# Kernel tuning notes

Measured on AMD Instinct MI355X. Metric: run time of the kernel, lower is better.

The kernel has to match this reference:

```python
import jax, jax.numpy as jnp
import numpy as np

B, T, C, H = 4, 1024, 768, 12
HD = C // H  # 64
EPS = 1e-5

def setup_inputs() -> dict:
    key = jax.random.key(0)
    ks = jax.random.split(key, 6)
    s = 0.02
    return {
        "x": jax.random.normal(ks[0], (B, T, C), jnp.float32),
        "ln1_w": jnp.ones((C,), jnp.float32),
        "w_attn": jax.random.normal(ks[1], (C, 3 * C), jnp.float32) * s,
        "w_pos": jax.random.normal(ks[2], (C, C), jnp.float32) * s,
        "w_cproj": jax.random.normal(ks[3], (C, C), jnp.float32) * s,
        "ln2_w": jnp.ones((C,), jnp.float32),
        "w_fc": jax.random.normal(ks[4], (C, 4 * C), jnp.float32) * s,
        "w_mproj": jax.random.normal(ks[5], (4 * C, C), jnp.float32) * s,
    }

def _layernorm(x, w):
    m = jnp.mean(x, axis=-1, keepdims=True)
    v = jnp.mean(jnp.square(x - m), axis=-1, keepdims=True)
    return (x - m) * jax.lax.rsqrt(v + EPS) * w

def _rpe_table(dtype):
    # sinusoidal table over relative distances [-(T-1), T-1] -> [2T-1, HD]
    inv_freq = 1.0 / (10000.0 ** (jnp.arange(0, HD, 2, dtype=jnp.float32) / HD))
    dist = jnp.arange(-(T - 1), T, dtype=jnp.float32)
    freqs = dist[:, None] * inv_freq[None, :]
    return jnp.concatenate([jnp.sin(freqs), jnp.cos(freqs)], axis=-1).astype(dtype)

def reference(x, ln1_w, w_attn, w_pos, w_cproj, ln2_w, w_fc, w_mproj):
    # ---- attention branch ----
    h = _layernorm(x, ln1_w)
    qkv = h @ w_attn                                 # [B,T,3C]
    q, k, v = jnp.split(qkv, 3, axis=-1)
    q = q.reshape(B, T, H, HD).transpose(0, 2, 1, 3)  # [B,H,T,HD]
    k = k.reshape(B, T, H, HD).transpose(0, 2, 1, 3)
    v = v.reshape(B, T, H, HD).transpose(0, 2, 1, 3)
    # note: the original also computes p = c_pos(x) but never uses it (dead code)

    # relative position embeddings gathered to [T,T,HD]
    idx = jnp.arange(T)
    rel = jnp.clip(idx[:, None] - idx[None, :], -(T - 1), T - 1) + (T - 1)
    rpe = _rpe_table(q.dtype)[rel]                    # [T,T,HD]

    scale = 1.0 / np.sqrt(HD)
    att = (jnp.einsum('bhid,bhjd->bhij', q, k)
           + jnp.einsum('bhid,ijd->bhij', q, rpe)) * scale
    causal = idx[:, None] >= idx[None, :]             # [T,T] lower-tri
    att = jnp.where(causal, att, -jnp.inf)
    att = jax.nn.softmax(att, axis=-1)
    y = jnp.einsum('bhij,bhjd->bhid', att, v)         # [B,H,T,HD]
    y = y.transpose(0, 2, 1, 3).reshape(B, T, C) @ w_cproj
    x = x + y

    # ---- MLP branch ----
    h2 = _layernorm(x, ln2_w)
    m = jax.nn.gelu(h2 @ w_fc, approximate=False) @ w_mproj
    return x + m
```

## Files before the change

kernel.cpp:

```cpp
#include <hip/hip_runtime.h>
#include <math.h>

typedef __attribute__((ext_vector_type(8))) short bf16x8;
typedef __attribute__((ext_vector_type(4))) float f32x4;
typedef __attribute__((ext_vector_type(16))) float f32x16;
typedef __attribute__((ext_vector_type(4))) unsigned u32x4;

__device__ inline short f2bf(float f) {
  unsigned u = __builtin_bit_cast(unsigned, f);
  u = u + 0x7fffu + ((u >> 16) & 1u);
  return (short)(u >> 16);
}
__device__ inline float bf2f(short s) {
  return __builtin_bit_cast(float, ((unsigned)(unsigned short)s) << 16);
}
__device__ inline unsigned cvt_pk_bf16(float lo, float hi) {
  unsigned r;
  asm("v_cvt_pk_bf16_f32 %0, %1, %2" : "=v"(r) : "v"(lo), "v"(hi));
  return r;
}

__device__ inline void gload16(const short* g, short* l) {
  __builtin_amdgcn_global_load_lds(
      (const __attribute__((address_space(1))) unsigned*)g,
      (__attribute__((address_space(3))) unsigned*)l, 16, 0, 0);
}

__global__ __launch_bounds__(256) void wtrans_all(
    const float* __restrict__ wa, const float* __restrict__ wc,
    const float* __restrict__ wf, const float* __restrict__ wm,
    short* __restrict__ oa, short* __restrict__ oc,
    short* __restrict__ of, short* __restrict__ om) {
  __shared__ float tile[32][33];
  int blk = blockIdx.x;
  const float* in; short* out; int K, N, bx;
  if (blk < 1728)      { in = wa; out = oa; K = 768;  N = 2304; bx = 72; }
  else if (blk < 2304) { blk -= 1728; in = wc; out = oc; K = 768;  N = 768;  bx = 24; }
  else if (blk < 4608) { blk -= 2304; in = wf; out = of; K = 768;  N = 3072; bx = 96; }
  else                 { blk -= 4608; in = wm; out = om; K = 3072; N = 768;  bx = 24; }
  const int n0 = (blk % bx) * 32, k0 = (blk / bx) * 32;
  const int tx = threadIdx.x & 31, ty = threadIdx.x >> 5;
  #pragma unroll
  for (int r = ty; r < 32; r += 8)
    tile[r][tx] = in[(size_t)(k0 + r) * N + n0 + tx];
  __syncthreads();
  #pragma unroll
  for (int r = ty; r < 32; r += 8)
    out[(size_t)(n0 + r) * K + k0 + tx] = f2bf(tile[tx][r]);
}

__global__ __launch_bounds__(256) void qprime_kernel(
    const short* __restrict__ qkv, short* __restrict__ qpr,
    short* __restrict__ ktab) {
  const int idx = blockIdx.x * 256 + threadIdx.x;
  const int cc = idx & 31;
  const int row = idx >> 5;
  const int i = row & 1023, bh = row >> 10;
  const int b = bh / 12, h = bh % 12;
  const float invf = exp2f(-(float)cc * (13.287712379549449f / 32.0f));
  const float ang = (float)i * invf;
  float si, co;
  __sincosf(ang, &si, &co);
  if (bh == 0) {
    ktab[i * 64 + cc]      = f2bf(co);
    ktab[i * 64 + 32 + cc] = f2bf(si);
  }
  const short* q = qkv + (size_t)(b * 1024 + i) * 2304 + h * 64;
  const float qs = bf2f(q[cc]), qc = bf2f(q[32 + cc]);
  qpr[(size_t)row * 64 + cc]      = f2bf(qs * si + qc * co);
  qpr[(size_t)row * 64 + 32 + cc] = f2bf(qc * si - qs * co);
}

__global__ __launch_bounds__(256) void ln_kernel(
    const float* __restrict__ x, const float* __restrict__ w,
    short* __restrict__ out) {
  const int row = blockIdx.x, tid = threadIdx.x;
  const float* xr = x + (size_t)row * 768;
  float v0 = xr[tid], v1 = xr[tid + 256], v2 = xr[tid + 512];
  float s = v0 + v1 + v2;
  #pragma unroll
  for (int o = 1; o < 64; o <<= 1) s += __shfl_xor(s, o);
  __shared__ float red[8];
  const int wv = tid >> 6;
  if ((tid & 63) == 0) red[wv] = s;
  __syncthreads();
  const float mean = (red[0] + red[1] + red[2] + red[3]) * (1.0f / 768.0f);
  v0 -= mean; v1 -= mean; v2 -= mean;
  float q = v0 * v0 + v1 * v1 + v2 * v2;
  #pragma unroll
  for (int o = 1; o < 64; o <<= 1) q += __shfl_xor(q, o);
  if ((tid & 63) == 0) red[4 + wv] = q;
  __syncthreads();
  const float var = (red[4] + red[5] + red[6] + red[7]) * (1.0f / 768.0f);
  const float inv = 1.0f / sqrtf(var + 1e-5f);
  out[(size_t)row * 768 + tid]       = f2bf(v0 * inv * w[tid]);
  out[(size_t)row * 768 + tid + 256] = f2bf(v1 * inv * w[tid + 256]);
  out[(size_t)row * 768 + tid + 512] = f2bf(v2 * inv * w[tid + 512]);
}

__global__ __launch_bounds__(256) void vtrans_kernel(
    const short* __restrict__ qkv, short* __restrict__ vT) {
  __shared__ short tile[64][65];
  const int blk = blockIdx.x;
  const int bh = blk >> 4, t0 = (blk & 15) * 64;
  const int b = bh / 12, h = bh % 12;
  const int tx = threadIdx.x & 63, ty = threadIdx.x >> 6;
  const short* src = qkv + (size_t)(b * 1024 + t0) * 2304 + 1536 + h * 64;
  #pragma unroll
  for (int r = ty; r < 64; r += 4)
    tile[r][tx] = src[(size_t)r * 2304 + tx];
  __syncthreads();
  short* dst = vT + (size_t)bh * 64 * 1024 + t0;
  #pragma unroll
  for (int r = ty; r < 64; r += 4)
    dst[(size_t)r * 1024 + tx] = tile[tx][r];
}

template <int EPI, int BM, int BN>
__global__ __launch_bounds__(256) void gemm_bt(
    const short* __restrict__ A, const short* __restrict__ Bt,
    const float* __restrict__ res, float* __restrict__ outF,
    short* __restrict__ outB, int M, int N, int K, int lda, int ldb) {
  __shared__ __align__(16) short As[2][BM * 32];
  __shared__ __align__(16) short Bs[2][BN * 32];
  constexpr int WM = BM / 2, WN = BN / 2;
  constexpr int MI = WM / 16, NJ = WN / 16;
  const int tid = threadIdx.x;
  const int w = tid >> 6, lane = tid & 63;
  const int m0 = blockIdx.y * BM, n0 = blockIdx.x * BN;
  const int wm = (w >> 1) * WM, wn = (w & 1) * WN;
  const int lr = lane >> 2;
  const int lc = (lane & 3) * 8;
  if constexpr (EPI == 3) {
    A += (size_t)blockIdx.z * K;
    Bt += (size_t)blockIdx.z * K;
    outF += (size_t)blockIdx.z * M * N;
  }
  f32x4 acc[MI][NJ];
  #pragma unroll
  for (int i = 0; i < MI; i++)
    #pragma unroll
    for (int j = 0; j < NJ; j++)
      #pragma unroll
      for (int r = 0; r < 4; r++) acc[i][j][r] = 0.0f;

  const int nt = K / 32;
  #pragma unroll
  for (int p = 0; p < BM / 64; ++p)
    gload16(A + (size_t)(m0 + p * 64 + w * 16 + lr) * lda + lc,
            &As[0][p * 2048 + w * 512]);
  #pragma unroll
  for (int p = 0; p < BN / 64; ++p)
    gload16(Bt + (size_t)(n0 + p * 64 + w * 16 + lr) * ldb + lc,
            &Bs[0][p * 2048 + w * 512]);
  __syncthreads();

  for (int t = 0; t < nt; ++t) {
    const int cur = t & 1;
    if (t + 1 < nt) {
      const int kt = (t + 1) * 32;
      #pragma unroll
      for (int p = 0; p < BM / 64; ++p)
        gload16(A + (size_t)(m0 + p * 64 + w * 16 + lr) * lda + kt + lc,
                &As[cur ^ 1][p * 2048 + w * 512]);
      #pragma unroll
      for (int p = 0; p < BN / 64; ++p)
        gload16(Bt + (size_t)(n0 + p * 64 + w * 16 + lr) * ldb + kt + lc,
                &Bs[cur ^ 1][p * 2048 + w * 512]);
    }
    bf16x8 af[MI], bfr[NJ];
    #pragma unroll
    for (int i = 0; i < MI; i++)
      af[i] = *(const bf16x8*)&As[cur][(wm + i * 16 + (lane & 15)) * 32 + (lane >> 4) * 8];
    #pragma unroll
    for (int j = 0; j < NJ; j++)
      bfr[j] = *(const bf16x8*)&Bs[cur][(wn + j * 16 + (lane & 15)) * 32 + (lane >> 4) * 8];
    #pragma unroll
    for (int i = 0; i < MI; i++)
      #pragma unroll
      for (int j = 0; j < NJ; j++)
        acc[i][j] = __builtin_amdgcn_mfma_f32_16x16x32_bf16(af[i], bfr[j],
                                                            acc[i][j], 0, 0, 0);
    __syncthreads();
  }
  const int r0 = (lane >> 4) * 4, cl = lane & 15;
  #pragma unroll
  for (int i = 0; i < MI; i++) {
    #pragma unroll
    for (int j = 0; j < NJ; j++) {
      const int gm = m0 + wm + i * 16 + r0;
      const int gn = n0 + wn + j * 16 + cl;
      #pragma unroll
      for (int r = 0; r < 4; r++) {
        const size_t idx = (size_t)(gm + r) * N + gn;
        const float v = acc[i][j][r];
        if constexpr (EPI == 0) {
          outB[idx] = f2bf(v);
        } else if constexpr (EPI == 1) {
          outF[idx] = res[idx] + v;
        } else if constexpr (EPI == 2) {
          outB[idx] = f2bf(0.5f * v * (1.0f + erff(v * 0.70710678118f)));
        } else {
          outF[idx] = v;
        }
      }
    }
  }
}

__global__ __launch_bounds__(256) void reduce_splitk(
    const float* __restrict__ Cp, const float* __restrict__ res,
    float* __restrict__ out) {
  const size_t i4 = ((size_t)blockIdx.x * 256 + threadIdx.x) * 4;
  float4 a = *(const float4*)(res + i4);
  #pragma unroll
  for (int z = 0; z < 2; ++z) {
    float4 p = *(const float4*)(Cp + (size_t)z * 3145728 + i4);
    a.x += p.x; a.y += p.y; a.z += p.z; a.w += p.w;
  }
  *(float4*)(out + i4) = a;
}

__global__ __launch_bounds__(512) void attn_part8(
    const short* __restrict__ qkv, const short* __restrict__ vT,
    const short* __restrict__ qpr, const short* __restrict__ ktab,
    float* __restrict__ mpart, float* __restrict__ lpart,
    short* __restrict__ Ypart) {
  const int tid = threadIdx.x;
  const int task = blockIdx.x * 8 + (tid >> 6);
  const int bh = task / 144;
  const int rem = task % 144;
  int c = 0;
  #pragma unroll
  for (int cc = 0; cc < 7; ++cc)
    if (rem >= 34 * (cc + 1) - 2 * (cc + 1) * (cc + 1)) c = cc + 1;
  const int it = 4 * c + (rem - (34 * c - 2 * c * c));
  const int b = bh / 12, h = bh % 12;
  const int I0 = it * 32;
  const int lane = tid & 63;
  const int li = lane & 31, hi = lane >> 5;
  constexpr float SCALE2 = 0.125f * 1.44269504089f;

  const short* qrow = qkv + (size_t)(b * 1024 + I0 + li) * 2304 + h * 64;
  const short* qprow = qpr + ((size_t)bh * 1024 + I0 + li) * 64;
  bf16x8 qf[8];
  #pragma unroll
  for (int s = 0; s < 4; s++) {
    qf[s]     = *(const bf16x8*)(qrow + s * 16 + hi * 8);
    qf[4 + s] = *(const bf16x8*)(qprow + s * 16 + hi * 8);
  }
  const short* kbase = qkv + (size_t)(b * 1024) * 2304 + 768 + h * 64;
  const short* vbase = vT + (size_t)bh * 64 * 1024;

  float m_run = -1e30f, l_run = 0.0f;
  f32x16 ya0, ya1;
  #pragma unroll
  for (int r = 0; r < 16; r++) { ya0[r] = 0.0f; ya1[r] = 0.0f; }

  const int jt0 = c * 4;
  const int jt1 = (c * 4 + 3 < it) ? (c * 4 + 3) : it;

  bf16x8 kn[8];
  {
    const short* kb = kbase + (size_t)(jt0 * 32 + li) * 2304;
    const short* kt = ktab + (size_t)(jt0 * 32 + li) * 64;
    #pragma unroll
    for (int s = 0; s < 4; s++) {
      kn[s]     = *(const bf16x8*)(kb + s * 16 + hi * 8);
      kn[4 + s] = *(const bf16x8*)(kt + s * 16 + hi * 8);
    }
  }

  for (int jt = jt0; jt <= jt1; ++jt) {
    const int J0 = jt * 32;
    bf16x8 kf[8];
    #pragma unroll
    for (int s = 0; s < 8; s++) kf[s] = kn[s];
    if (jt < jt1) {
      const short* kb = kbase + (size_t)((jt + 1) * 32 + li) * 2304;
      const short* kt = ktab + (size_t)((jt + 1) * 32 + li) * 64;
      #pragma unroll
      for (int s = 0; s < 4; s++) {
        kn[s]     = *(const bf16x8*)(kb + s * 16 + hi * 8);
        kn[4 + s] = *(const bf16x8*)(kt + s * 16 + hi * 8);
      }
    }
    bf16x8 vc[4];
    #pragma unroll
    for (int s = 0; s < 2; s++) {
      vc[s * 2]     = *(const bf16x8*)(vbase + (size_t)li * 1024 + J0 + s * 16 + hi * 8);
      vc[s * 2 + 1] = *(const bf16x8*)(vbase + (size_t)(32 + li) * 1024 + J0 + s * 16 + hi * 8);
    }
    f32x16 sa0, sa1;
    #pragma unroll
    for (int r = 0; r < 16; r++) { sa0[r] = 0.0f; sa1[r] = 0.0f; }
    __builtin_amdgcn_s_setprio(1);
    #pragma unroll
    for (int s = 0; s < 4; s++) {
      sa0 = __builtin_amdgcn_mfma_f32_32x32x16_bf16(kf[2 * s],     qf[2 * s],     sa0, 0, 0, 0);
      sa1 = __builtin_amdgcn_mfma_f32_32x32x16_bf16(kf[2 * s + 1], qf[2 * s + 1], sa1, 0, 0, 0);
    }
    __builtin_amdgcn_s_setprio(0);
    float sv[16];
    float mx = -1e30f;
    if (jt == it) {
      #pragma unroll
      for (int r = 0; r < 16; r++) {
        const int j = (r & 3) + 8 * (r >> 2) + 4 * hi;
        float v = (sa0[r] + sa1[r]) * SCALE2;
        v = (j <= li) ? v : -1e30f;
        sv[r] = v;
        mx = fmaxf(mx, v);
      }
    } else {
      #pragma unroll
      for (int r = 0; r < 16; r++) {
        const float v = (sa0[r] + sa1[r]) * SCALE2;
        sv[r] = v;
        mx = fmaxf(mx, v);
      }
    }
    mx = fmaxf(mx, __shfl_xor(mx, 32));
    float mref = m_run;
    float alpha = 1.0f;
    const bool resc = !__all(mx <= m_run + 11.5f);
    if (resc) {
      mref = fmaxf(m_run, mx);
      alpha = exp2f(m_run - mref);
      m_run = mref;
    }
    float psum = 0.0f;
    unsigned pw[8];
    #pragma unroll
    for (int t = 0; t < 8; t++) {
      const float p0 = exp2f(sv[2 * t] - mref);
      const float p1 = exp2f(sv[2 * t + 1] - mref);
      psum += p0 + p1;
      pw[t] = cvt_pk_bf16(p0, p1);
    }
    psum += __shfl_xor(psum, 32);
    l_run = l_run * alpha + psum;
    if (resc) {
      #pragma unroll
      for (int r = 0; r < 16; r++) {
        const int row = (r & 3) + 8 * (r >> 2) + 4 * hi;
        const float a = __shfl(alpha, row);
        ya0[r] *= a;
        ya1[r] *= a;
      }
    }
    #pragma unroll
    for (int s = 0; s < 2; s++) {
      unsigned a0 = pw[4 * s],     b0 = pw[4 * s + 2];
      unsigned a1 = pw[4 * s + 1], b1 = pw[4 * s + 3];
      asm volatile("v_permlane32_swap_b32 %0, %1" : "+v"(a0), "+v"(b0));
      asm volatile("v_permlane32_swap_b32 %0, %1" : "+v"(a1), "+v"(b1));
      u32x4 t4;
      t4[0] = a0; t4[1] = a1; t4[2] = b0; t4[3] = b1;
      const bf16x8 pf = __builtin_bit_cast(bf16x8, t4);
      __builtin_amdgcn_s_setprio(1);
      ya0 = __builtin_amdgcn_mfma_f32_32x32x16_bf16(pf, vc[s * 2],     ya0, 0, 0, 0);
      ya1 = __builtin_amdgcn_mfma_f32_32x32x16_bf16(pf, vc[s * 2 + 1], ya1, 0, 0, 0);
      __builtin_amdgcn_s_setprio(0);
    }
  }
  if (hi == 0) {
    mpart[(size_t)task * 32 + li] = m_run;
    lpart[(size_t)task * 32 + li] = l_run;
  }
  short* yb = Ypart + (size_t)task * 2048;
  #pragma unroll
  for (int r = 0; r < 16; r++) {
    const int row = (r & 3) + 8 * (r >> 2) + 4 * hi;
    yb[row * 64 + li]      = f2bf(ya0[r]);
    yb[row * 64 + 32 + li] = f2bf(ya1[r]);
  }
}

__global__ __launch_bounds__(256) void attn_combine(
    const float* __restrict__ mpart, const float* __restrict__ lpart,
    const short* __restrict__ Ypart, short* __restrict__ yout) {
  const int blk = blockIdx.x;
  const int it = blk & 31, bh = blk >> 5;
  const int b = bh / 12, h = bh % 12;
  const int g = it >> 2;
  const int nc = g + 1;
  const int row = threadIdx.x >> 3;
  const int c0 = (threadIdx.x & 7) * 8;
  float mv[8], lv[8], wgt[8];
  float m = -1e30f;
  #pragma unroll
  for (int cI = 0; cI < 8; ++cI) {
    const int idx = bh * 144 + it + 30 * cI - 2 * cI * cI;
    mv[cI] = (cI < nc) ? mpart[(size_t)idx * 32 + row] : -1e30f;
    lv[cI] = (cI < nc) ? lpart[(size_t)idx * 32 + row] : 0.0f;
    m = fmaxf(m, mv[cI]);
  }
  float L = 0.0f;
  #pragma unroll
  for (int cI = 0; cI < 8; ++cI) {
    wgt[cI] = exp2f(mv[cI] - m);
    L += lv[cI] * wgt[cI];
  }
  const float inv = 1.0f / L;
  float y[8];
  #pragma unroll
  for (int r = 0; r < 8; r++) y[r] = 0.0f;
  #pragma unroll
  for (int cI = 0; cI < 8; ++cI) {
    if (cI < nc) {
      const int idx = bh * 144 + it + 30 * cI - 2 * cI * cI;
      bf16x8 v = *(const bf16x8*)(Ypart + ((size_t)idx * 32 + row) * 64 + c0);
      #pragma unroll
      for (int r = 0; r < 8; r++) y[r] += bf2f(v[r]) * wgt[cI];
    }
  }
  short* dst = yout + (size_t)(b * 1024 + it * 32 + row) * 768 + h * 64 + c0;
  #pragma unroll
  for (int r = 0; r < 8; r++) dst[r] = f2bf(y[r] * inv);
}

extern "C" void kernel_launch(void* const* d_in, const int* in_sizes, int n_in,
                              void* d_out, int out_size, void* d_ws, size_t ws_size,
                              hipStream_t stream) {
  const float* x       = (const float*)d_in[0];
  const float* ln1_w   = (const float*)d_in[1];
  const float* w_attn  = (const float*)d_in[2];
  const float* w_cproj = (const float*)d_in[4];
  const float* ln2_w   = (const float*)d_in[5];
  const float* w_fc    = (const float*)d_in[6];
  const float* w_mproj = (const float*)d_in[7];
  float* out = (float*)d_out;
  char* ws = (char*)d_ws;

  short* wT_attn  = (short*)(ws + 0);
  short* wT_cproj = (short*)(ws + 3538944);
  short* wT_fc    = (short*)(ws + 4718592);
  short* wT_mproj = (short*)(ws + 9437184);
  short* ktab     = (short*)(ws + 14155776);
  short* h_bf     = (short*)(ws + 14417920);
  short* qpr      = (short*)(ws + 14417920);
  short* qkv_bf   = (short*)(ws + 20709376);
  short* vT       = (short*)(ws + 39583744);
  short* y_att    = (short*)(ws + 45875200);
  short* h2_bf    = (short*)(ws + 52166656);
  short* hfc_bf   = (short*)(ws + 58458112);
  float* mpart = (float*)(ws + 52166656);
  float* lpart = (float*)(ws + 53051392);
  short* Ypart = (short*)(ws + 53936128);
  float* Cpart = (float*)(ws + 20709376);

  wtrans_all<<<6912, 256, 0, stream>>>(w_attn, w_cproj, w_fc, w_mproj,
                                       wT_attn, wT_cproj, wT_fc, wT_mproj);

  ln_kernel<<<4096, 256, 0, stream>>>(x, ln1_w, h_bf);
  gemm_bt<0, 128, 128><<<dim3(18, 32), 256, 0, stream>>>(
      h_bf, wT_attn, nullptr, nullptr, qkv_bf, 4096, 2304, 768, 768, 768);
  qprime_kernel<<<6144, 256, 0, stream>>>(qkv_bf, qpr, ktab);
  vtrans_kernel<<<768, 256, 0, stream>>>(qkv_bf, vT);
  attn_part8<<<864, 512, 0, stream>>>(qkv_bf, vT, qpr, ktab, mpart, lpart, Ypart);
  attn_combine<<<1536, 256, 0, stream>>>(mpart, lpart, Ypart, y_att);
  gemm_bt<1, 64, 64><<<dim3(12, 64), 256, 0, stream>>>(
      y_att, wT_cproj, x, out, nullptr, 4096, 768, 768, 768, 768);
  ln_kernel<<<4096, 256, 0, stream>>>(out, ln2_w, h2_bf);
  gemm_bt<2, 128, 128><<<dim3(24, 32), 256, 0, stream>>>(
      h2_bf, wT_fc, nullptr, nullptr, hfc_bf, 4096, 3072, 768, 768, 768);
  gemm_bt<3, 128, 64><<<dim3(12, 32, 2), 256, 0, stream>>>(
      hfc_bf, wT_mproj, nullptr, Cpart, nullptr, 4096, 768, 1536, 3072, 3072);
  reduce_splitk<<<3072, 256, 0, stream>>>(Cpart, out, out);
}
```

Baseline: 228.2 us.

## Share K/V chunk tiles across waves via double-buffered LDS in attention partials

Reorganizes attn_part8 so each 8-wave block handles query tiles that share the same key chunk. The block cooperatively loads each 32-key K/ktab and V tile into double-buffered shared memory instead of every wave loading its own copy from global memory. Task mapping changes to 20 blocks per (b,h) with some idle waves, and the grid grows from 864 to 960 blocks. The cost is extra __syncthreads per key tile, imbalance when waves have differing causal work, and more LDS use per block.

```diff
diff --git a/kernel.cpp b/kernel.cpp
--- a/kernel.cpp
+++ b/kernel.cpp
@@ -226,20 +226,47 @@
     const short* __restrict__ qpr, const short* __restrict__ ktab,
     float* __restrict__ mpart, float* __restrict__ lpart,
     short* __restrict__ Ypart) {
+  __shared__ __align__(16) short Ka[2][32 * 136];
+  __shared__ __align__(16) short Va[2][64 * 40];
+  const int bx = blockIdx.x;
+  const int bh = bx / 20;
+  const int r = bx % 20;
+  int c, sub;
+  if (r < 4)        { c = 0; sub = r; }
+  else if (r < 8)   { c = 1; sub = r - 4; }
+  else if (r < 11)  { c = 2; sub = r - 8; }
+  else if (r < 14)  { c = 3; sub = r - 11; }
+  else if (r < 16)  { c = 4; sub = r - 14; }
+  else if (r < 18)  { c = 5; sub = r - 16; }
+  else if (r == 18) { c = 6; sub = 0; }
+  else              { c = 7; sub = 0; }
   const int tid = threadIdx.x;
-  const int task = blockIdx.x * 8 + (tid >> 6);
-  const int bh = task / 144;
-  const int rem = task % 144;
-  int c = 0;
-  #pragma unroll
-  for (int cc = 0; cc < 7; ++cc)
-    if (rem >= 34 * (cc + 1) - 2 * (cc + 1) * (cc + 1)) c = cc + 1;
-  const int it = 4 * c + (rem - (34 * c - 2 * c * c));
-  const int b = bh / 12, h = bh % 12;
-  const int I0 = it * 32;
+  const int w = tid >> 6;
   const int lane = tid & 63;
   const int li = lane & 31, hi = lane >> 5;
+  const int it = 4 * c + sub * 8 + w;
+  const bool valid = (it <= 31);
+  const int b = bh / 12, h = bh % 12;
+  const int I0 = (valid ? it : 31) * 32;
+  const int jt0 = 4 * c;
+  const int jtmax = valid ? ((it < jt0 + 3) ? it : jt0 + 3) : (jt0 - 1);
   constexpr float SCALE2 = 0.125f * 1.44269504089f;
+
+  const short* kbase = qkv + (size_t)(b * 1024) * 2304 + 768 + h * 64;
+  const short* vbase = vT + (size_t)bh * 64 * 1024;
+
+  const int krow = tid >> 4, kch = tid & 15;
+  const short* ksrc = (kch < 8) ? (kbase + kch * 8) : (ktab + (kch - 8) * 8);
+  const size_t kstr = (kch < 8) ? 2304 : 64;
+  const int vrow = tid >> 2, vch = tid & 3;
+
+  int4 kreg, vreg;
+  {
+    const int J0 = jt0 * 32;
+    kreg = *(const int4*)(ksrc + (size_t)(J0 + krow) * kstr);
+    if (tid < 256)
+      vreg = *(const int4*)(vbase + (size_t)vrow * 1024 + J0 + vch * 8);
+  }
 
   const short* qrow = qkv + (size_t)(b * 1024 + I0 + li) * 2304 + h * 64;
   const short* qprow = qpr + ((size_t)bh * 1024 + I0 + li) * 64;
@@ -249,131 +276,127 @@
     qf[s]     = *(const bf16x8*)(qrow + s * 16 + hi * 8);
     qf[4 + s] = *(const bf16x8*)(qprow + s * 16 + hi * 8);
   }
-  const short* kbase = qkv + (size_t)(b * 1024) * 2304 + 768 + h * 64;
-  const short* vbase = vT + (size_t)bh * 64 * 1024;
+
+  *(int4*)&Ka[0][krow * 136 + kch * 8] = kreg;
+  if (tid < 256) *(int4*)&Va[0][vrow * 40 + vch * 8] = vreg;
+  __syncthreads();
 
   float m_run = -1e30f, l_run = 0.0f;
   f32x16 ya0, ya1;
   #pragma unroll
-  for (int r = 0; r < 16; r++) { ya0[r] = 0.0f; ya1[r] = 0.0f; }
-
-  const int jt0 = c * 4;
-  const int jt1 = (c * 4 + 3 < it) ? (c * 4 + 3) : it;
-
-  bf16x8 kn[8];
-  {
-    const short* kb = kbase + (size_t)(jt0 * 32 + li) * 2304;
-    const short* kt = ktab + (size_t)(jt0 * 32 + li) * 64;
-    #pragma unroll
-    for (int s = 0; s < 4; s++) {
-      kn[s]     = *(const bf16x8*)(kb + s * 16 + hi * 8);
-      kn[4 + s] = *(const bf16x8*)(kt + s * 16 + hi * 8);
-    }
-  }
-
-  for (int jt = jt0; jt <= jt1; ++jt) {
-    const int J0 = jt * 32;
-    bf16x8 kf[8];
-    #pragma unroll
-    for (int s = 0; s < 8; s++) kf[s] = kn[s];
-    if (jt < jt1) {
-      const short* kb = kbase + (size_t)((jt + 1) * 32 + li) * 2304;
-      const short* kt = ktab + (size_t)((jt + 1) * 32 + li) * 64;
+  for (int q = 0; q < 16; q++) { ya0[q] = 0.0f; ya1[q] = 0.0f; }
+
+  for (int t = 0; t < 4; ++t) {
+    const int cur = t & 1;
+    if (t < 3) {
+      const int J0n = (jt0 + t + 1) * 32;
+      kreg = *(const int4*)(ksrc + (size_t)(J0n + krow) * kstr);
+      if (tid < 256)
+        vreg = *(const int4*)(vbase + (size_t)vrow * 1024 + J0n + vch * 8);
+    }
+    const int jt = jt0 + t;
+    if (jt <= jtmax) {
+      bf16x8 kf[8];
+      #pragma unroll
+      for (int s = 0; s < 8; s++)
+        kf[s] = *(const bf16x8*)&Ka[cur][li * 136 + s * 16 + hi * 8];
+      bf16x8 vc[4];
+      #pragma unroll
+      for (int s = 0; s < 2; s++) {
+        vc[s * 2]     = *(const bf16x8*)&Va[cur][li * 40 + s * 16 + hi * 8];
+        vc[s * 2 + 1] = *(const bf16x8*)&Va[cur][(32 + li) * 40 + s * 16 + hi * 8];
+      }
+      f32x16 sa0, sa1;
+      #pragma unroll
+      for (int q = 0; q < 16; q++) { sa0[q] = 0.0f; sa1[q] = 0.0f; }
+      __builtin_amdgcn_s_setprio(1);
       #pragma unroll
       for (int s = 0; s < 4; s++) {
-        kn[s]     = *(const bf16x8*)(kb + s * 16 + hi * 8);
-        kn[4 + s] = *(const bf16x8*)(kt + s * 16 + hi * 8);
-      }
-    }
-    bf16x8 vc[4];
-    #pragma unroll
-    for (int s = 0; s < 2; s++) {
-      vc[s * 2]     = *(const bf16x8*)(vbase + (size_t)li * 1024 + J0 + s * 16 + hi * 8);
-      vc[s * 2 + 1] = *(const bf16x8*)(vbase + (size_t)(32 + li) * 1024 + J0 + s * 16 + hi * 8);
-    }
-    f32x16 sa0, sa1;
-    #pragma unroll
-    for (int r = 0; r < 16; r++) { sa0[r] = 0.0f; sa1[r] = 0.0f; }
-    __builtin_amdgcn_s_setprio(1);
-    #pragma unroll
-    for (int s = 0; s < 4; s++) {
-      sa0 = __builtin_amdgcn_mfma_f32_32x32x16_bf16(kf[2 * s],     qf[2 * s],     sa0, 0, 0, 0);
-      sa1 = __builtin_amdgcn_mfma_f32_32x32x16_bf16(kf[2 * s + 1], qf[2 * s + 1], sa1, 0, 0, 0);
-    }
-    __builtin_amdgcn_s_setprio(0);
-    float sv[16];
-    float mx = -1e30f;
-    if (jt == it) {
-      #pragma unroll
-      for (int r = 0; r < 16; r++) {
-        const int j = (r & 3) + 8 * (r >> 2) + 4 * hi;
-        float v = (sa0[r] + sa1[r]) * SCALE2;
-        v = (j <= li) ? v : -1e30f;
-        sv[r] = v;
-        mx = fmaxf(mx, v);
-      }
-    } else {
-      #pragma unroll
-      for (int r = 0; r < 16; r++) {
-        const float v = (sa0[r] + sa1[r]) * SCALE2;
-        sv[r] = v;
-        mx = fmaxf(mx, v);
-      }
-    }
-    mx = fmaxf(mx, __shfl_xor(mx, 32));
-    float mref = m_run;
-    float alpha = 1.0f;
-    const bool resc = !__all(mx <= m_run + 11.5f);
-    if (resc) {
-      mref = fmaxf(m_run, mx);
-      alpha = exp2f(m_run - mref);
-      m_run = mref;
-    }
-    float psum = 0.0f;
-    unsigned pw[8];
-    #pragma unroll
-    for (int t = 0; t < 8; t++) {
-      const float p0 = exp2f(sv[2 * t] - mref);
-      const float p1 = exp2f(sv[2 * t + 1] - mref);
-      psum += p0 + p1;
-      pw[t] = cvt_pk_bf16(p0, p1);
-    }
-    psum += __shfl_xor(psum, 32);
-    l_run = l_run * alpha + psum;
-    if (resc) {
-      #pragma unroll
-      for (int r = 0; r < 16; r++) {
-        const int row = (r & 3) + 8 * (r >> 2) + 4 * hi;
-        const float a = __shfl(alpha, row);
-        ya0[r] *= a;
-        ya1[r] *= a;
-      }
-    }
-    #pragma unroll
-    for (int s = 0; s < 2; s++) {
-      unsigned a0 = pw[4 * s],     b0 = pw[4 * s + 2];
-      unsigned a1 = pw[4 * s + 1], b1 = pw[4 * s + 3];
-      asm volatile("v_permlane32_swap_b32 %0, %1" : "+v"(a0), "+v"(b0));
-      asm volatile("v_permlane32_swap_b32 %0, %1" : "+v"(a1), "+v"(b1));
-      u32x4 t4;
-      t4[0] = a0; t4[1] = a1; t4[2] = b0; t4[3] = b1;
-      const bf16x8 pf = __builtin_bit_cast(bf16x8, t4);
-      __builtin_amdgcn_s_setprio(1);
-      ya0 = __builtin_amdgcn_mfma_f32_32x32x16_bf16(pf, vc[s * 2],     ya0, 0, 0, 0);
-      ya1 = __builtin_amdgcn_mfma_f32_32x32x16_bf16(pf, vc[s * 2 + 1], ya1, 0, 0, 0);
+        sa0 = __builtin_amdgcn_mfma_f32_32x32x16_bf16(kf[2 * s],     qf[2 * s],     sa0, 0, 0, 0);
+        sa1 = __builtin_amdgcn_mfma_f32_32x32x16_bf16(kf[2 * s + 1], qf[2 * s + 1], sa1, 0, 0, 0);
+      }
       __builtin_amdgcn_s_setprio(0);
-    }
-  }
+      float sv[16];
+      float mx = -1e30f;
+      if (jt == it) {
+        #pragma unroll
+        for (int q = 0; q < 16; q++) {
+          const int j = (q & 3) + 8 * (q >> 2) + 4 * hi;
+          float v = (sa0[q] + sa1[q]) * SCALE2;
+          v = (j <= li) ? v : -1e30f;
+          sv[q] = v;
+          mx = fmaxf(mx, v);
+        }
+      } else {
+        #pragma unroll
+        for (int q = 0; q < 16; q++) {
+          const float v = (sa0[q] + sa1[q]) * SCALE2;
+          sv[q] = v;
+          mx = fmaxf(mx, v);
+        }
+      }
+      mx = fmaxf(mx, __shfl_xor(mx, 32));
+      float mref = m_run;
+      float alpha = 1.0f;
+      const bool resc = !__all(mx <= m_run + 11.5f);
+      if (resc) {
+        mref = fmaxf(m_run, mx);
+        alpha = exp2f(m_run - mref);
+        m_run = mref;
+      }
+      float psum = 0.0f;
+      unsigned pw[8];
+      #pragma unroll
+      for (int q = 0; q < 8; q++) {
+        const float p0 = exp2f(sv[2 * q] - mref);
+        const float p1 = exp2f(sv[2 * q + 1] - mref);
+        psum += p0 + p1;
+        pw[q] = cvt_pk_bf16(p0, p1);
+      }
+      psum += __shfl_xor(psum, 32);
+      l_run = l_run * alpha + psum;
+      if (resc) {
+        #pragma unroll
+        for (int q = 0; q < 16; q++) {
+          const int row = (q & 3) + 8 * (q >> 2) + 4 * hi;
+          const float a = __shfl(alpha, row);
+          ya0[q] *= a;
+          ya1[q] *= a;
+        }
+      }
+      #pragma unroll
+      for (int s = 0; s < 2; s++) {
+        unsigned a0 = pw[4 * s],     b0 = pw[4 * s + 2];
+        unsigned a1 = pw[4 * s + 1], b1 = pw[4 * s + 3];
+        asm volatile("v_permlane32_swap_b32 %0, %1" : "+v"(a0), "+v"(b0));
+        asm volatile("v_permlane32_swap_b32 %0, %1" : "+v"(a1), "+v"(b1));
+        u32x4 t4;
+        t4[0] = a0; t4[1] = a1; t4[2] = b0; t4[3] = b1;
+        const bf16x8 pf = __builtin_bit_cast(bf16x8, t4);
+        __builtin_amdgcn_s_setprio(1);
+        ya0 = __builtin_amdgcn_mfma_f32_32x32x16_bf16(pf, vc[s * 2],     ya0, 0, 0, 0);
+        ya1 = __builtin_amdgcn_mfma_f32_32x32x16_bf16(pf, vc[s * 2 + 1], ya1, 0, 0, 0);
+        __builtin_amdgcn_s_setprio(0);
+      }
+    }
+    if (t < 3) {
+      *(int4*)&Ka[cur ^ 1][krow * 136 + kch * 8] = kreg;
+      if (tid < 256) *(int4*)&Va[cur ^ 1][vrow * 40 + vch * 8] = vreg;
+    }
+    __syncthreads();
+  }
+  if (!valid) return;
+  const int task = bh * 144 + it + 30 * c - 2 * c * c;
   if (hi == 0) {
     mpart[(size_t)task * 32 + li] = m_run;
     lpart[(size_t)task * 32 + li] = l_run;
   }
   short* yb = Ypart + (size_t)task * 2048;
   #pragma unroll
-  for (int r = 0; r < 16; r++) {
-    const int row = (r & 3) + 8 * (r >> 2) + 4 * hi;
-    yb[row * 64 + li]      = f2bf(ya0[r]);
-    yb[row * 64 + 32 + li] = f2bf(ya1[r]);
+  for (int q = 0; q < 16; q++) {
+    const int row = (q & 3) + 8 * (q >> 2) + 4 * hi;
+    yb[row * 64 + li]      = f2bf(ya0[q]);
+    yb[row * 64 + 32 + li] = f2bf(ya1[q]);
   }
 }
 
@@ -458,7 +481,7 @@
       h_bf, wT_attn, nullptr, nullptr, qkv_bf, 4096, 2304, 768, 768, 768);
   qprime_kernel<<<6144, 256, 0, stream>>>(qkv_bf, qpr, ktab);
   vtrans_kernel<<<768, 256, 0, stream>>>(qkv_bf, vT);
-  attn_part8<<<864, 512, 0, stream>>>(qkv_bf, vT, qpr, ktab, mpart, lpart, Ypart);
+  attn_part8<<<960, 512, 0, stream>>>(qkv_bf, vT, qpr, ktab, mpart, lpart, Ypart);
   attn_combine<<<1536, 256, 0, stream>>>(mpart, lpart, Ypart, y_att);
   gemm_bt<1, 64, 64><<<dim3(12, 64), 256, 0, stream>>>(
       y_att, wT_cproj, x, out, nullptr, 4096, 768, 768, 768, 768);
```

After: 208.0 us. 1.1x faster.
